# Performance work log

Measured on AMD Instinct MI355X. Metric: run time of the kernel, lower is better.

The kernel has to match this reference:

```python
import jax, jax.numpy as jnp
import numpy as np
import math

B, M, V, C, HID, BIN, H, W = 2, 1024, 300, 128, 128, 256, 384, 512


def fibonacci_sphere(n):
    # generate_grasp_views: n approximately-uniform directions on the unit sphere
    i = np.arange(n, dtype=np.float64)
    phi = (np.sqrt(5.0) - 1.0) / 2.0
    z = (2.0 * i + 1.0) / n - 1.0
    r = np.sqrt(np.maximum(1.0 - z * z, 0.0))
    t = 2.0 * np.pi * i * phi
    v = np.stack([r * np.cos(t), r * np.sin(t), z], -1)
    return (v / np.linalg.norm(v, axis=-1, keepdims=True)).astype(np.float32)


def setup_inputs():
    key = jax.random.key(0)
    ks = jax.random.split(key, 24)
    seed_features = jax.random.normal(ks[0], (B, C, M), jnp.float32)
    token_sel_idx = jax.random.randint(ks[1], (B, M), 0, H * W)
    fx = 525.0
    Kmat = jnp.array([[fx, 0.0, W / 2.0], [0.0, fx, H / 2.0], [0.0, 0.0, 1.0]], jnp.float32)
    K = jnp.broadcast_to(Kmat, (B, 3, 3))
    depth_map = 0.2 + 0.8 * jax.random.uniform(ks[2], (B, 1, H, W), jnp.float32)
    depth_prob = jax.nn.softmax(jax.random.normal(ks[3], (B, BIN, H, W), jnp.float32), axis=1)
    view_dirs = jnp.asarray(fibonacci_sphere(V))

    def lin(k, fan_in, shape):
        s = 1.0 / np.sqrt(fan_in)
        return jax.random.uniform(k, shape, jnp.float32, -s, s)

    qin = C + 7  # seed_feat + ray(3) + normal(3) + uncert(1)
    params = dict(
        Wq1=lin(ks[4], qin, (qin, HID)), bq1=lin(ks[5], qin, (HID,)),
        Wq2=lin(ks[6], HID, (HID, HID)), bq2=lin(ks[7], HID, (HID,)),
        Wa1=lin(ks[8], 3, (3, HID)), ba1=lin(ks[9], 3, (HID,)),
        Wa2=lin(ks[10], HID, (HID, HID)), ba2=lin(ks[11], HID, (HID,)),
        Wb1=lin(ks[12], 3, (3, HID // 2)), bb1=lin(ks[13], 3, (HID // 2,)),
        Wb2=lin(ks[14], HID // 2, (HID // 2, 1)), bb2=lin(ks[15], HID // 2, (1,)),
        Wr1=lin(ks[16], HID, (HID, C)), br1=lin(ks[17], HID, (C,)),
        Wr2=lin(ks[18], C, (C, C)), br2=lin(ks[19], C, (C,)),
    )
    return dict(seed_features=seed_features, token_sel_idx=token_sel_idx, K=K,
                depth_map=depth_map, depth_prob=depth_prob, view_dirs=view_dirs, **params)


def _views_to_rot(views):
    # batch_viewpoint_params_to_matrix(-views, angle=0)
    axis_x = -views
    zero = jnp.zeros_like(axis_x[..., 0])
    axis_y = jnp.stack([-axis_x[..., 1], axis_x[..., 0], zero], -1)
    ny = jnp.linalg.norm(axis_y, axis=-1, keepdims=True)
    fallback = jnp.broadcast_to(jnp.array([0.0, 1.0, 0.0], views.dtype), axis_y.shape)
    axis_y = jnp.where(ny < 1e-8, fallback, axis_y / jnp.maximum(ny, 1e-8))
    axis_x = axis_x / jnp.maximum(jnp.linalg.norm(axis_x, axis=-1, keepdims=True), 1e-8)
    axis_z = jnp.cross(axis_x, axis_y)
    return jnp.stack([axis_x, axis_y, axis_z], -1)  # (B,M,3,3)


def _forward(seed_features, token_sel_idx, K, depth_map, depth_prob, view_dirs,
             Wq1, bq1, Wq2, bq2, Wa1, ba1, Wa2, ba2, Wb1, bb1, Wb2, bb2, Wr1, br1, Wr2, br2):
    depth_map = jax.lax.stop_gradient(depth_map)   # .detach() in torch
    depth_prob = jax.lax.stop_gradient(depth_prob)
    # --- backproject depth to xyz map (B,3,H,W) ---
    ys, xs = jnp.meshgrid(jnp.arange(H, dtype=jnp.float32), jnp.arange(W, dtype=jnp.float32), indexing='ij')
    fx = K[:, 0, 0][:, None, None, None]; fy = K[:, 1, 1][:, None, None, None]
    cx = K[:, 0, 2][:, None, None, None]; cy = K[:, 1, 2][:, None, None, None]
    z = depth_map
    x = (xs[None, None] - cx) / fx * z
    y = (ys[None, None] - cy) / fy * z
    xyz = jnp.concatenate([x, y, z], axis=1)
    # --- central-difference normal map with replicate pad ---
    dx = (xyz[:, :, :, 2:] - xyz[:, :, :, :-2])[:, :, 1:-1, :]
    dy = (xyz[:, :, 2:, :] - xyz[:, :, :-2, :])[:, :, :, 1:-1]
    n = jnp.cross(dx.transpose(0, 2, 3, 1), dy.transpose(0, 2, 3, 1))
    n = n / jnp.maximum(jnp.linalg.norm(n, axis=-1, keepdims=True), 1e-6)
    normal_map = jnp.pad(n.transpose(0, 3, 1, 2), ((0, 0), (0, 0), (1, 1), (1, 1)), mode='edge')
    # --- depth uncertainty: normalized entropy over bins ---
    p = jnp.maximum(depth_prob, 1e-8)
    uncert_map = jnp.clip(-(p * jnp.log(p)).sum(axis=1, keepdims=True) / math.log(BIN), 0.0, 1.0)
    # --- per-seed irregular gathers ---
    def gather(feat, idx):
        Bf, Cf = feat.shape[0], feat.shape[1]
        flat = feat.reshape(Bf, Cf, H * W)
        return jnp.take_along_axis(flat, jnp.broadcast_to(idx[:, None, :], (Bf, Cf, idx.shape[1])), axis=2)
    normal_bm3 = gather(normal_map, token_sel_idx).transpose(0, 2, 1)  # (B,M,3)
    uncert_bm1 = gather(uncert_map, token_sel_idx).transpose(0, 2, 1)  # (B,M,1)
    u = (token_sel_idx % W).astype(jnp.float32)
    v = (token_sel_idx // W).astype(jnp.float32)
    rx = (u - K[:, 0, 2][:, None]) / K[:, 0, 0][:, None]
    ry = (v - K[:, 1, 2][:, None]) / K[:, 1, 1][:, None]
    rays = jnp.stack([rx, ry, jnp.ones_like(rx)], -1)
    rays = rays / jnp.maximum(jnp.linalg.norm(rays, axis=-1, keepdims=True), 1e-12)
    normal_bm3 = normal_bm3 * (1.0 - uncert_bm1)
    # --- query / anchor / bias MLPs ---
    q_in = jnp.concatenate([seed_features.transpose(0, 2, 1), rays, normal_bm3, uncert_bm1], -1)
    q = jax.nn.relu(jax.nn.relu(q_in @ Wq1 + bq1) @ Wq2 + bq2)          # (B,M,HID)
    a = jax.nn.relu(view_dirs @ Wa1 + ba1) @ Wa2 + ba2                  # (V,HID)
    bias = (jax.nn.relu(view_dirs @ Wb1 + bb1) @ Wb2 + bb2)[:, 0]        # (V,)
    logits = jnp.einsum('bmh,vh->bmv', q, a) / jnp.sqrt(jnp.float32(HID)) + bias
    view_score = jax.nn.sigmoid(logits)                                  # (B,M,V)
    # --- top-1 view selection + gather xyz / rot / anchor feat ---
    top_inds = jnp.argmax(view_score, axis=-1)                           # (B,M)
    top_xyz = view_dirs[top_inds]                                        # (B,M,3)
    rot = _views_to_rot(top_xyz)                                         # (B,M,3,3)
    top_a = a[top_inds]                                                  # (B,M,HID)
    res = jax.nn.relu((q + top_a) @ Wr1 + br1) @ Wr2 + br2               # (B,M,C)
    res_feat = res.transpose(0, 2, 1)                                    # (B,C,M)
    return view_score, top_inds, top_xyz, rot, res_feat


def reference(seed_features, token_sel_idx, K, depth_map, depth_prob, view_dirs,
              Wq1, bq1, Wq2, bq2, Wa1, ba1, Wa2, ba2, Wb1, bb1, Wb2, bb2, Wr1, br1, Wr2, br2):
    return _forward(seed_features, token_sel_idx, K, depth_map, depth_prob, view_dirs,
                    Wq1, bq1, Wq2, bq2, Wa1, ba1, Wa2, ba2, Wb1, bb1, Wb2, bb2, Wr1, br1, Wr2, br2)
```

## Files before the change

### kernel.cpp

```cpp
#include <hip/hip_runtime.h>
#include <math.h>

#define B 2
#define M 1024
#define V 300
#define C 128
#define HID 128
#define BIN 256
#define H 384
#define W 512
#define QIN (C + 7)

__global__ __launch_bounds__(128) void transpose_seed(
    const float* __restrict__ in, float* __restrict__ out) {
  __shared__ float tile[32][33];
  const int b  = blockIdx.z;
  const int c0 = blockIdx.x * 32;
  const int m0 = blockIdx.y * 32;
  const int tx = threadIdx.x;
#pragma unroll
  for (int r = threadIdx.y; r < 32; r += 4)
    tile[r][tx] = in[((size_t)b * C + c0 + r) * M + m0 + tx];
  __syncthreads();
#pragma unroll
  for (int r = threadIdx.y; r < 32; r += 4)
    out[((size_t)b * M + m0 + r) * C + c0 + tx] = tile[tx][r];
}

__global__ __launch_bounds__(HID) void anchor_kernel(
    const float* __restrict__ view_dirs,
    const float* __restrict__ Wa1, const float* __restrict__ ba1,
    const float* __restrict__ Wa2, const float* __restrict__ ba2,
    const float* __restrict__ Wb1, const float* __restrict__ bb1,
    const float* __restrict__ Wb2, const float* __restrict__ bb2,
    float* __restrict__ a_out, float* __restrict__ aT_out,
    float* __restrict__ bias_out) {
  const int v = blockIdx.x;
  const int t = threadIdx.x;
  __shared__ float h1[HID];

  const float vd0 = view_dirs[v * 3 + 0];
  const float vd1 = view_dirs[v * 3 + 1];
  const float vd2 = view_dirs[v * 3 + 2];

  float h = vd0 * Wa1[0 * HID + t] + vd1 * Wa1[1 * HID + t] + vd2 * Wa1[2 * HID + t] + ba1[t];
  h1[t] = fmaxf(h, 0.0f);

  if (t < 64) {
    float x = vd0 * Wb1[0 * 64 + t] + vd1 * Wb1[1 * 64 + t] + vd2 * Wb1[2 * 64 + t] + bb1[t];
    x = fmaxf(x, 0.0f) * Wb2[t];
#pragma unroll
    for (int o = 32; o > 0; o >>= 1) x += __shfl_down(x, o, 64);
    if (t == 0) bias_out[v] = x + bb2[0];
  }
  __syncthreads();

  float acc = ba2[t];
#pragma unroll 8
  for (int k = 0; k < HID; ++k) acc += h1[k] * Wa2[k * HID + t];
  a_out[v * HID + t] = acc;
  aT_out[(size_t)t * V + v] = acc;
}

__global__ __launch_bounds__(128) void seed_kernel(
    const float* __restrict__ seedT, const int* __restrict__ token_sel_idx,
    const float* __restrict__ Kmat, const float* __restrict__ depth_map,
    const float* __restrict__ depth_prob, const float* __restrict__ view_dirs,
    const float* __restrict__ Wq1, const float* __restrict__ bq1,
    const float* __restrict__ Wq2, const float* __restrict__ bq2,
    const float* __restrict__ Wr1, const float* __restrict__ br1,
    const float* __restrict__ Wr2, const float* __restrict__ br2,
    const float* __restrict__ a_ws, const float* __restrict__ aT_ws,
    const float* __restrict__ bias_ws,
    float* __restrict__ out_view_score, float* __restrict__ out_top_inds,
    float* __restrict__ out_top_xyz, float* __restrict__ out_rot,
    float* __restrict__ out_res) {
  const int bm = blockIdx.x;
  const int b = bm / M;
  const int m = bm - b * M;
  const int t = threadIdx.x;
  const int lane = t & 63;
  const int wv = t >> 6;

  __shared__ float qin_s[QIN + 1];
  __shared__ float hs[HID];
  __shared__ float qs[HID];
  __shared__ float atop_s[HID];
  __shared__ float ered[2];
  __shared__ float wbv[2];
  __shared__ int   wbi[2];
  __shared__ int   sbest;

  qin_s[t] = seedT[((size_t)b * M + m) * C + t];

  const int idx = token_sel_idx[b * M + m];

  {
    const float* dp = depth_prob + (size_t)b * BIN * H * W + idx;
    float p0 = fmaxf(dp[(size_t)(2 * t + 0) * (H * W)], 1e-8f);
    float p1 = fmaxf(dp[(size_t)(2 * t + 1) * (H * W)], 1e-8f);
    float e = p0 * logf(p0) + p1 * logf(p1);
#pragma unroll
    for (int o = 32; o > 0; o >>= 1) e += __shfl_down(e, o, 64);
    if (lane == 0) ered[wv] = e;
  }
  __syncthreads();

  if (t == 0) {
    float uncert = (-(ered[0] + ered[1])) / 5.5451774444795623f;
    uncert = fminf(fmaxf(uncert, 0.0f), 1.0f);

    const float fx = Kmat[b * 9 + 0], fy = Kmat[b * 9 + 4];
    const float cx = Kmat[b * 9 + 2], cy = Kmat[b * 9 + 5];
    const int w = idx % W;
    const int h = idx / W;
    const int hc = min(max(h, 1), H - 2);
    const int wc = min(max(w, 1), W - 2);

    const float* dm = depth_map + (size_t)b * H * W;
    const float zl = dm[hc * W + (wc - 1)];
    const float zr = dm[hc * W + (wc + 1)];
    const float zu = dm[(hc - 1) * W + wc];
    const float zd = dm[(hc + 1) * W + wc];

    const float dxx = (wc + 1 - cx) / fx * zr - (wc - 1 - cx) / fx * zl;
    const float dxy = (hc - cy) / fy * zr - (hc - cy) / fy * zl;
    const float dxz = zr - zl;
    const float dyx = (wc - cx) / fx * zd - (wc - cx) / fx * zu;
    const float dyy = (hc + 1 - cy) / fy * zd - (hc - 1 - cy) / fy * zu;
    const float dyz = zd - zu;

    float nx = dxy * dyz - dxz * dyy;
    float ny = dxz * dyx - dxx * dyz;
    float nz = dxx * dyy - dxy * dyx;
    const float nn = fmaxf(sqrtf(nx * nx + ny * ny + nz * nz), 1e-6f);
    const float sc = (1.0f - uncert) / nn;

    const float rx = ((float)w - cx) / fx;
    const float ry = ((float)h - cy) / fy;
    const float rn = fmaxf(sqrtf(rx * rx + ry * ry + 1.0f), 1e-12f);

    qin_s[128] = rx / rn;
    qin_s[129] = ry / rn;
    qin_s[130] = 1.0f / rn;
    qin_s[131] = nx * sc;
    qin_s[132] = ny * sc;
    qin_s[133] = nz * sc;
    qin_s[134] = uncert;
  }
  __syncthreads();

  float acc = bq1[t];
#pragma unroll 5
  for (int i = 0; i < QIN; ++i) acc += qin_s[i] * Wq1[i * HID + t];
  hs[t] = fmaxf(acc, 0.0f);
  __syncthreads();

  acc = bq2[t];
#pragma unroll 8
  for (int k = 0; k < HID; ++k) acc += hs[k] * Wq2[k * HID + t];
  qs[t] = fmaxf(acc, 0.0f);
  __syncthreads();

  const int col2 = 256 + (t < 44 ? t : 43);
  float d0 = 0.0f, d1 = 0.0f, d2 = 0.0f;
#pragma unroll 8
  for (int k = 0; k < HID; ++k) {
    const float qk = qs[k];
    const float* row = aT_ws + (size_t)k * V;
    d0 += qk * row[t];
    d1 += qk * row[t + 128];
    d2 += qk * row[col2];
  }
  const float rsq = 0.08838834764831845f;
  const float sc0 = 1.0f / (1.0f + expf(-(d0 * rsq + bias_ws[t])));
  const float sc1 = 1.0f / (1.0f + expf(-(d1 * rsq + bias_ws[t + 128])));
  const float sc2 = 1.0f / (1.0f + expf(-(d2 * rsq + bias_ws[col2])));

  float* vs_out = out_view_score + (size_t)bm * V;
  vs_out[t] = sc0;
  vs_out[t + 128] = sc1;
  if (t < 44) vs_out[t + 256] = sc2;

  float bv = sc0; int bi = t;
  if (sc1 > bv) { bv = sc1; bi = t + 128; }
  if (t < 44 && sc2 > bv) { bv = sc2; bi = t + 256; }
#pragma unroll
  for (int o = 32; o > 0; o >>= 1) {
    const float ov = __shfl_down(bv, o, 64);
    const int oi = __shfl_down(bi, o, 64);
    if (ov > bv || (ov == bv && oi < bi)) { bv = ov; bi = oi; }
  }
  if (lane == 0) { wbv[wv] = bv; wbi[wv] = bi; }
  __syncthreads();

  if (t == 0) {
    float fbv = wbv[0]; int fbi = wbi[0];
    if (wbv[1] > fbv || (wbv[1] == fbv && wbi[1] < fbi)) { fbv = wbv[1]; fbi = wbi[1]; }
    sbest = fbi;

    out_top_inds[bm] = (float)fbi;
    const float vx = view_dirs[fbi * 3 + 0];
    const float vy = view_dirs[fbi * 3 + 1];
    const float vz = view_dirs[fbi * 3 + 2];
    out_top_xyz[(size_t)bm * 3 + 0] = vx;
    out_top_xyz[(size_t)bm * 3 + 1] = vy;
    out_top_xyz[(size_t)bm * 3 + 2] = vz;

    float ax0 = -vx, ax1 = -vy, ax2 = -vz;
    float ay0 = vy, ay1 = -vx, ay2 = 0.0f;
    const float nyn = sqrtf(ay0 * ay0 + ay1 * ay1);
    if (nyn < 1e-8f) {
      ay0 = 0.0f; ay1 = 1.0f; ay2 = 0.0f;
    } else {
      const float d = fmaxf(nyn, 1e-8f);
      ay0 /= d; ay1 /= d;
    }
    const float an = fmaxf(sqrtf(ax0 * ax0 + ax1 * ax1 + ax2 * ax2), 1e-8f);
    ax0 /= an; ax1 /= an; ax2 /= an;
    const float az0 = ax1 * ay2 - ax2 * ay1;
    const float az1 = ax2 * ay0 - ax0 * ay2;
    const float az2 = ax0 * ay1 - ax1 * ay0;
    float* R = out_rot + (size_t)bm * 9;
    R[0] = ax0; R[1] = ay0; R[2] = az0;
    R[3] = ax1; R[4] = ay1; R[5] = az1;
    R[6] = ax2; R[7] = ay2; R[8] = az2;
  }
  __syncthreads();
  const int best = sbest;

  atop_s[t] = a_ws[best * HID + t];
  __syncthreads();

  float racc = br1[t];
#pragma unroll 8
  for (int k = 0; k < HID; ++k) racc += (qs[k] + atop_s[k]) * Wr1[k * HID + t];
  hs[t] = fmaxf(racc, 0.0f);
  __syncthreads();

  racc = br2[t];
#pragma unroll 8
  for (int k = 0; k < HID; ++k) racc += hs[k] * Wr2[k * HID + t];
  out_res[((size_t)b * C + t) * M + m] = racc;
}

extern "C" void kernel_launch(void* const* d_in, const int* in_sizes, int n_in,
                              void* d_out, int out_size, void* d_ws, size_t ws_size,
                              hipStream_t stream) {
  const float* seed  = (const float*)d_in[0];
  const int*   tok   = (const int*)d_in[1];
  const float* Km    = (const float*)d_in[2];
  const float* dmap  = (const float*)d_in[3];
  const float* dprob = (const float*)d_in[4];
  const float* vdirs = (const float*)d_in[5];
  const float* Wq1 = (const float*)d_in[6];  const float* bq1 = (const float*)d_in[7];
  const float* Wq2 = (const float*)d_in[8];  const float* bq2 = (const float*)d_in[9];
  const float* Wa1 = (const float*)d_in[10]; const float* ba1 = (const float*)d_in[11];
  const float* Wa2 = (const float*)d_in[12]; const float* ba2 = (const float*)d_in[13];
  const float* Wb1 = (const float*)d_in[14]; const float* bb1 = (const float*)d_in[15];
  const float* Wb2 = (const float*)d_in[16]; const float* bb2 = (const float*)d_in[17];
  const float* Wr1 = (const float*)d_in[18]; const float* br1 = (const float*)d_in[19];
  const float* Wr2 = (const float*)d_in[20]; const float* br2 = (const float*)d_in[21];

  float* out = (float*)d_out;
  float* vs  = out;
  float* ti  = vs + (size_t)B * M * V;
  float* tx  = ti + (size_t)B * M;
  float* rot = tx + (size_t)B * M * 3;
  float* rf  = rot + (size_t)B * M * 9;

  float* a_ws    = (float*)d_ws;
  float* aT_ws   = a_ws + (size_t)V * HID;
  float* bias_ws = aT_ws + (size_t)HID * V;
  float* seedT   = bias_ws + V;

  transpose_seed<<<dim3(C / 32, M / 32, B), dim3(32, 4), 0, stream>>>(seed, seedT);
  anchor_kernel<<<V, HID, 0, stream>>>(vdirs, Wa1, ba1, Wa2, ba2, Wb1, bb1, Wb2, bb2,
                                       a_ws, aT_ws, bias_ws);
  seed_kernel<<<B * M, 128, 0, stream>>>(seedT, tok, Km, dmap, dprob, vdirs,
                                         Wq1, bq1, Wq2, bq2, Wr1, br1, Wr2, br2,
                                         a_ws, aT_ws, bias_ws, vs, ti, tx, rot, rf);
}
```

Before: 551.2 us.

## Process four seeds per block to reuse weight loads and drop transpose kernel

The seed kernel now handles four seeds per block, so each weight and anchor element loaded from global memory is reused across four MLP rows held in registers. Shared-memory activations are read as float4, and the output residual is written as a float4 across the four seeds. The separate transpose kernel is removed: seed features are read directly as float4 along the M dimension. The cost is more registers per thread and a quarter as many blocks, which may reduce occupancy and latency hiding for the scattered depth_prob gathers.

```diff
diff --git a/kernel.cpp b/kernel.cpp
--- a/kernel.cpp
+++ b/kernel.cpp
@@ -10,22 +10,7 @@
 #define H 384
 #define W 512
 #define QIN (C + 7)
-
-__global__ __launch_bounds__(128) void transpose_seed(
-    const float* __restrict__ in, float* __restrict__ out) {
-  __shared__ float tile[32][33];
-  const int b  = blockIdx.z;
-  const int c0 = blockIdx.x * 32;
-  const int m0 = blockIdx.y * 32;
-  const int tx = threadIdx.x;
-#pragma unroll
-  for (int r = threadIdx.y; r < 32; r += 4)
-    tile[r][tx] = in[((size_t)b * C + c0 + r) * M + m0 + tx];
-  __syncthreads();
-#pragma unroll
-  for (int r = threadIdx.y; r < 32; r += 4)
-    out[((size_t)b * M + m0 + r) * C + c0 + tx] = tile[tx][r];
-}
+#define G 4
 
 __global__ __launch_bounds__(HID) void anchor_kernel(
     const float* __restrict__ view_dirs,
@@ -63,7 +48,7 @@
 }
 
 __global__ __launch_bounds__(128) void seed_kernel(
-    const float* __restrict__ seedT, const int* __restrict__ token_sel_idx,
+    const float* __restrict__ seed, const int* __restrict__ token_sel_idx,
     const float* __restrict__ Kmat, const float* __restrict__ depth_map,
     const float* __restrict__ depth_prob, const float* __restrict__ view_dirs,
     const float* __restrict__ Wq1, const float* __restrict__ bq1,
@@ -75,39 +60,58 @@
     float* __restrict__ out_view_score, float* __restrict__ out_top_inds,
     float* __restrict__ out_top_xyz, float* __restrict__ out_rot,
     float* __restrict__ out_res) {
-  const int bm = blockIdx.x;
-  const int b = bm / M;
-  const int m = bm - b * M;
+  const int s0 = blockIdx.x * G;
+  const int b = s0 >> 10;
+  const int m0 = s0 & (M - 1);
   const int t = threadIdx.x;
   const int lane = t & 63;
   const int wv = t >> 6;
 
-  __shared__ float qin_s[QIN + 1];
-  __shared__ float hs[HID];
-  __shared__ float qs[HID];
-  __shared__ float atop_s[HID];
-  __shared__ float ered[2];
-  __shared__ float wbv[2];
-  __shared__ int   wbi[2];
-  __shared__ int   sbest;
-
-  qin_s[t] = seedT[((size_t)b * M + m) * C + t];
-
-  const int idx = token_sel_idx[b * M + m];
-
-  {
-    const float* dp = depth_prob + (size_t)b * BIN * H * W + idx;
-    float p0 = fmaxf(dp[(size_t)(2 * t + 0) * (H * W)], 1e-8f);
-    float p1 = fmaxf(dp[(size_t)(2 * t + 1) * (H * W)], 1e-8f);
-    float e = p0 * logf(p0) + p1 * logf(p1);
-#pragma unroll
-    for (int o = 32; o > 0; o >>= 1) e += __shfl_down(e, o, 64);
-    if (lane == 0) ered[wv] = e;
-  }
-  __syncthreads();
-
-  if (t == 0) {
-    float uncert = (-(ered[0] + ered[1])) / 5.5451774444795623f;
+  __shared__ __align__(16) float qin_s[G][136];
+  __shared__ __align__(16) float hs[G][HID];
+  __shared__ __align__(16) float qs[G][HID];
+  __shared__ __align__(16) float sum_s[G][HID];
+  __shared__ float ered[G][2];
+  __shared__ float wbv[G][2];
+  __shared__ int   wbi[G][2];
+  __shared__ int   sbest[G];
+  __shared__ int   sidx[G];
+
+  if (t < G) sidx[t] = token_sel_idx[b * M + m0 + t];
+
+  {
+    const float4 sv = *(const float4*)&seed[((size_t)b * C + t) * M + m0];
+    qin_s[0][t] = sv.x; qin_s[1][t] = sv.y; qin_s[2][t] = sv.z; qin_s[3][t] = sv.w;
+  }
+  if (t < G) qin_s[t][135] = 0.0f;
+  __syncthreads();
+
+  {
+    const size_t HW = (size_t)H * W;
+    float e[G];
+#pragma unroll
+    for (int g = 0; g < G; ++g) {
+      const float* dp = depth_prob + (size_t)b * BIN * HW + sidx[g];
+      const float p0 = fmaxf(dp[(size_t)(2 * t + 0) * HW], 1e-8f);
+      const float p1 = fmaxf(dp[(size_t)(2 * t + 1) * HW], 1e-8f);
+      e[g] = p0 * logf(p0) + p1 * logf(p1);
+    }
+#pragma unroll
+    for (int o = 32; o > 0; o >>= 1) {
+#pragma unroll
+      for (int g = 0; g < G; ++g) e[g] += __shfl_down(e[g], o, 64);
+    }
+    if (lane == 0) {
+#pragma unroll
+      for (int g = 0; g < G; ++g) ered[g][wv] = e[g];
+    }
+  }
+  __syncthreads();
+
+  if (t < G) {
+    const int g = t;
+    const int idx = sidx[g];
+    float uncert = (-(ered[g][0] + ered[g][1])) / 5.5451774444795623f;
     uncert = fminf(fmaxf(uncert, 0.0f), 1.0f);
 
     const float fx = Kmat[b * 9 + 0], fy = Kmat[b * 9 + 4];
@@ -140,65 +144,132 @@
     const float ry = ((float)h - cy) / fy;
     const float rn = fmaxf(sqrtf(rx * rx + ry * ry + 1.0f), 1e-12f);
 
-    qin_s[128] = rx / rn;
-    qin_s[129] = ry / rn;
-    qin_s[130] = 1.0f / rn;
-    qin_s[131] = nx * sc;
-    qin_s[132] = ny * sc;
-    qin_s[133] = nz * sc;
-    qin_s[134] = uncert;
-  }
-  __syncthreads();
-
-  float acc = bq1[t];
-#pragma unroll 5
-  for (int i = 0; i < QIN; ++i) acc += qin_s[i] * Wq1[i * HID + t];
-  hs[t] = fmaxf(acc, 0.0f);
-  __syncthreads();
-
-  acc = bq2[t];
-#pragma unroll 8
-  for (int k = 0; k < HID; ++k) acc += hs[k] * Wq2[k * HID + t];
-  qs[t] = fmaxf(acc, 0.0f);
+    qin_s[g][128] = rx / rn;
+    qin_s[g][129] = ry / rn;
+    qin_s[g][130] = 1.0f / rn;
+    qin_s[g][131] = nx * sc;
+    qin_s[g][132] = ny * sc;
+    qin_s[g][133] = nz * sc;
+    qin_s[g][134] = uncert;
+  }
+  __syncthreads();
+
+  {
+    float acc[G];
+    const float b1 = bq1[t];
+#pragma unroll
+    for (int g = 0; g < G; ++g) acc[g] = b1;
+    for (int i0 = 0; i0 < 132; i0 += 4) {
+      const float w0 = Wq1[(i0 + 0) * HID + t];
+      const float w1 = Wq1[(i0 + 1) * HID + t];
+      const float w2 = Wq1[(i0 + 2) * HID + t];
+      const float w3 = Wq1[(i0 + 3) * HID + t];
+#pragma unroll
+      for (int g = 0; g < G; ++g) {
+        const float4 qv = *(const float4*)&qin_s[g][i0];
+        acc[g] += qv.x * w0 + qv.y * w1 + qv.z * w2 + qv.w * w3;
+      }
+    }
+    {
+      const float w0 = Wq1[132 * HID + t];
+      const float w1 = Wq1[133 * HID + t];
+      const float w2 = Wq1[134 * HID + t];
+#pragma unroll
+      for (int g = 0; g < G; ++g) {
+        const float4 qv = *(const float4*)&qin_s[g][132];
+        acc[g] += qv.x * w0 + qv.y * w1 + qv.z * w2;
+      }
+    }
+#pragma unroll
+    for (int g = 0; g < G; ++g) hs[g][t] = fmaxf(acc[g], 0.0f);
+  }
+  __syncthreads();
+
+  {
+    float acc[G];
+    const float b2 = bq2[t];
+#pragma unroll
+    for (int g = 0; g < G; ++g) acc[g] = b2;
+    for (int k0 = 0; k0 < HID; k0 += 4) {
+      const float w0 = Wq2[(k0 + 0) * HID + t];
+      const float w1 = Wq2[(k0 + 1) * HID + t];
+      const float w2 = Wq2[(k0 + 2) * HID + t];
+      const float w3 = Wq2[(k0 + 3) * HID + t];
+#pragma unroll
+      for (int g = 0; g < G; ++g) {
+        const float4 hv = *(const float4*)&hs[g][k0];
+        acc[g] += hv.x * w0 + hv.y * w1 + hv.z * w2 + hv.w * w3;
+      }
+    }
+#pragma unroll
+    for (int g = 0; g < G; ++g) qs[g][t] = fmaxf(acc[g], 0.0f);
+  }
   __syncthreads();
 
   const int col2 = 256 + (t < 44 ? t : 43);
-  float d0 = 0.0f, d1 = 0.0f, d2 = 0.0f;
-#pragma unroll 8
-  for (int k = 0; k < HID; ++k) {
-    const float qk = qs[k];
-    const float* row = aT_ws + (size_t)k * V;
-    d0 += qk * row[t];
-    d1 += qk * row[t + 128];
-    d2 += qk * row[col2];
-  }
+  float d0[G], d1[G], d2[G];
+#pragma unroll
+  for (int g = 0; g < G; ++g) { d0[g] = 0.0f; d1[g] = 0.0f; d2[g] = 0.0f; }
+  for (int k0 = 0; k0 < HID; k0 += 4) {
+    const float* r0 = aT_ws + (size_t)(k0 + 0) * V;
+    const float* r1 = aT_ws + (size_t)(k0 + 1) * V;
+    const float* r2 = aT_ws + (size_t)(k0 + 2) * V;
+    const float* r3 = aT_ws + (size_t)(k0 + 3) * V;
+    const float a00 = r0[t], a01 = r0[t + 128], a02 = r0[col2];
+    const float a10 = r1[t], a11 = r1[t + 128], a12 = r1[col2];
+    const float a20 = r2[t], a21 = r2[t + 128], a22 = r2[col2];
+    const float a30 = r3[t], a31 = r3[t + 128], a32 = r3[col2];
+#pragma unroll
+    for (int g = 0; g < G; ++g) {
+      const float4 qv = *(const float4*)&qs[g][k0];
+      d0[g] += qv.x * a00 + qv.y * a10 + qv.z * a20 + qv.w * a30;
+      d1[g] += qv.x * a01 + qv.y * a11 + qv.z * a21 + qv.w * a31;
+      d2[g] += qv.x * a02 + qv.y * a12 + qv.z * a22 + qv.w * a32;
+    }
+  }
+
   const float rsq = 0.08838834764831845f;
-  const float sc0 = 1.0f / (1.0f + expf(-(d0 * rsq + bias_ws[t])));
-  const float sc1 = 1.0f / (1.0f + expf(-(d1 * rsq + bias_ws[t + 128])));
-  const float sc2 = 1.0f / (1.0f + expf(-(d2 * rsq + bias_ws[col2])));
-
-  float* vs_out = out_view_score + (size_t)bm * V;
-  vs_out[t] = sc0;
-  vs_out[t + 128] = sc1;
-  if (t < 44) vs_out[t + 256] = sc2;
-
-  float bv = sc0; int bi = t;
-  if (sc1 > bv) { bv = sc1; bi = t + 128; }
-  if (t < 44 && sc2 > bv) { bv = sc2; bi = t + 256; }
+  const float bw0 = bias_ws[t];
+  const float bw1 = bias_ws[t + 128];
+  const float bw2 = bias_ws[col2];
+  float bv[G]; int bi[G];
+#pragma unroll
+  for (int g = 0; g < G; ++g) {
+    const float sc0 = 1.0f / (1.0f + expf(-(d0[g] * rsq + bw0)));
+    const float sc1 = 1.0f / (1.0f + expf(-(d1[g] * rsq + bw1)));
+    const float sc2 = 1.0f / (1.0f + expf(-(d2[g] * rsq + bw2)));
+
+    float* vs_out = out_view_score + (size_t)(b * M + m0 + g) * V;
+    vs_out[t] = sc0;
+    vs_out[t + 128] = sc1;
+    if (t < 44) vs_out[t + 256] = sc2;
+
+    bv[g] = sc0; bi[g] = t;
+    if (sc1 > bv[g]) { bv[g] = sc1; bi[g] = t + 128; }
+    if (t < 44 && sc2 > bv[g]) { bv[g] = sc2; bi[g] = t + 256; }
+  }
 #pragma unroll
   for (int o = 32; o > 0; o >>= 1) {
-    const float ov = __shfl_down(bv, o, 64);
-    const int oi = __shfl_down(bi, o, 64);
-    if (ov > bv || (ov == bv && oi < bi)) { bv = ov; bi = oi; }
-  }
-  if (lane == 0) { wbv[wv] = bv; wbi[wv] = bi; }
-  __syncthreads();
-
-  if (t == 0) {
-    float fbv = wbv[0]; int fbi = wbi[0];
-    if (wbv[1] > fbv || (wbv[1] == fbv && wbi[1] < fbi)) { fbv = wbv[1]; fbi = wbi[1]; }
-    sbest = fbi;
-
+#pragma unroll
+    for (int g = 0; g < G; ++g) {
+      const float ov = __shfl_down(bv[g], o, 64);
+      const int oi = __shfl_down(bi[g], o, 64);
+      if (ov > bv[g] || (ov == bv[g] && oi < bi[g])) { bv[g] = ov; bi[g] = oi; }
+    }
+  }
+  if (lane == 0) {
+#pragma unroll
+    for (int g = 0; g < G; ++g) { wbv[g][wv] = bv[g]; wbi[g][wv] = bi[g]; }
+  }
+  __syncthreads();
+
+  if (t < G) {
+    const int g = t;
+    float fbv = wbv[g][0]; int fbi = wbi[g][0];
+    if (wbv[g][1] > fbv || (wbv[g][1] == fbv && wbi[g][1] < fbi)) { fbv = wbv[g][1]; fbi = wbi[g][1]; }
+    sbest[g] = fbi;
+
+    const int bm = b * M + m0 + g;
     out_top_inds[bm] = (float)fbi;
     const float vx = view_dirs[fbi * 3 + 0];
     const float vy = view_dirs[fbi * 3 + 1];
@@ -227,21 +298,52 @@
     R[6] = ax2; R[7] = ay2; R[8] = az2;
   }
   __syncthreads();
-  const int best = sbest;
-
-  atop_s[t] = a_ws[best * HID + t];
-  __syncthreads();
-
-  float racc = br1[t];
-#pragma unroll 8
-  for (int k = 0; k < HID; ++k) racc += (qs[k] + atop_s[k]) * Wr1[k * HID + t];
-  hs[t] = fmaxf(racc, 0.0f);
-  __syncthreads();
-
-  racc = br2[t];
-#pragma unroll 8
-  for (int k = 0; k < HID; ++k) racc += hs[k] * Wr2[k * HID + t];
-  out_res[((size_t)b * C + t) * M + m] = racc;
+
+#pragma unroll
+  for (int g = 0; g < G; ++g) sum_s[g][t] = qs[g][t] + a_ws[sbest[g] * HID + t];
+  __syncthreads();
+
+  {
+    float acc[G];
+    const float b1 = br1[t];
+#pragma unroll
+    for (int g = 0; g < G; ++g) acc[g] = b1;
+    for (int k0 = 0; k0 < HID; k0 += 4) {
+      const float w0 = Wr1[(k0 + 0) * HID + t];
+      const float w1 = Wr1[(k0 + 1) * HID + t];
+      const float w2 = Wr1[(k0 + 2) * HID + t];
+      const float w3 = Wr1[(k0 + 3) * HID + t];
+#pragma unroll
+      for (int g = 0; g < G; ++g) {
+        const float4 sv = *(const float4*)&sum_s[g][k0];
+        acc[g] += sv.x * w0 + sv.y * w1 + sv.z * w2 + sv.w * w3;
+      }
+    }
+#pragma unroll
+    for (int g = 0; g < G; ++g) hs[g][t] = fmaxf(acc[g], 0.0f);
+  }
+  __syncthreads();
+
+  {
+    float acc[G];
+    const float b2 = br2[t];
+#pragma unroll
+    for (int g = 0; g < G; ++g) acc[g] = b2;
+    for (int k0 = 0; k0 < HID; k0 += 4) {
+      const float w0 = Wr2[(k0 + 0) * HID + t];
+      const float w1 = Wr2[(k0 + 1) * HID + t];
+      const float w2 = Wr2[(k0 + 2) * HID + t];
+      const float w3 = Wr2[(k0 + 3) * HID + t];
+#pragma unroll
+      for (int g = 0; g < G; ++g) {
+        const float4 hv = *(const float4*)&hs[g][k0];
+        acc[g] += hv.x * w0 + hv.y * w1 + hv.z * w2 + hv.w * w3;
+      }
+    }
+    float4 o;
+    o.x = acc[0]; o.y = acc[1]; o.z = acc[2]; o.w = acc[3];
+    *(float4*)&out_res[((size_t)b * C + t) * M + m0] = o;
+  }
 }
 
 extern "C" void kernel_launch(void* const* d_in, const int* in_sizes, int n_in,
@@ -272,12 +374,10 @@
   float* a_ws    = (float*)d_ws;
   float* aT_ws   = a_ws + (size_t)V * HID;
   float* bias_ws = aT_ws + (size_t)HID * V;
-  float* seedT   = bias_ws + V;
-
-  transpose_seed<<<dim3(C / 32, M / 32, B), dim3(32, 4), 0, stream>>>(seed, seedT);
+
   anchor_kernel<<<V, HID, 0, stream>>>(vdirs, Wa1, ba1, Wa2, ba2, Wb1, bb1, Wb2, bb2,
                                        a_ws, aT_ws, bias_ws);
-  seed_kernel<<<B * M, 128, 0, stream>>>(seedT, tok, Km, dmap, dprob, vdirs,
-                                         Wq1, bq1, Wq2, bq2, Wr1, br1, Wr2, br2,
-                                         a_ws, aT_ws, bias_ws, vs, ti, tx, rot, rf);
+  seed_kernel<<<(B * M) / G, 128, 0, stream>>>(seed, tok, Km, dmap, dprob, vdirs,
+                                               Wq1, bq1, Wq2, bq2, Wr1, br1, Wr2, br2,
+                                               a_ws, aT_ws, bias_ws, vs, ti, tx, rot, rf);
 }
```

Result: no change. 544.6 us (-1.2%).
